# Kernel optimization log

Hardware: AMD Instinct MI355X
Metric: run time of the kernel (lower is better)

## Reference

```python
import jax, jax.numpy as jnp
import numpy as np

B, NV, NT = 256, 64, 77
UNIT_DIM, PROJ_DIM, V_HID, T_HID = 512, 512, 768, 512
TEMP_INIT = 0.07
LN_EPS = 1e-5
NORM_EPS = 1e-12


def _xavier(key, fan_in, fan_out):
    lim = np.sqrt(6.0 / (fan_in + fan_out))
    return jax.random.uniform(key, (fan_in, fan_out), jnp.float32, -lim, lim)


def _ln(x, g, b):
    mu = jnp.mean(x, axis=-1, keepdims=True)
    var = jnp.mean(jnp.square(x - mu), axis=-1, keepdims=True)
    return (x - mu) * jax.lax.rsqrt(var + LN_EPS) * g + b


def _l2norm(x):
    n = jnp.sqrt(jnp.sum(jnp.square(x), axis=-1, keepdims=True))
    return x / jnp.maximum(n, NORM_EPS)


def _unit_mlp(x, W1, b1, g, bt, W2, b2):
    # Linear -> LayerNorm -> GELU(exact) -> Linear
    h = x @ W1 + b1
    h = jax.nn.gelu(_ln(h, g, bt), approximate=False)
    return h @ W2 + b2


def setup_inputs() -> dict:
    key = jax.random.key(0)
    ks = jax.random.split(key, 12)
    inp = {
        'visual_units': jax.random.normal(ks[0], (B, NV, UNIT_DIM), jnp.float32),
        'text_units': jax.random.normal(ks[1], (B, NT, UNIT_DIM), jnp.float32),
        'visual_cls': jax.random.normal(ks[2], (B, V_HID), jnp.float32),
        'text_cls': jax.random.normal(ks[3], (B, T_HID), jnp.float32),
        # visual unit proj
        'vW1': _xavier(ks[4], UNIT_DIM, PROJ_DIM), 'vb1': jnp.zeros(PROJ_DIM),
        'vg': jnp.ones(PROJ_DIM), 'vbt': jnp.zeros(PROJ_DIM),
        'vW2': _xavier(ks[5], PROJ_DIM, PROJ_DIM), 'vb2': jnp.zeros(PROJ_DIM),
        # text unit proj
        'tW1': _xavier(ks[6], UNIT_DIM, PROJ_DIM), 'tb1': jnp.zeros(PROJ_DIM),
        'tg': jnp.ones(PROJ_DIM), 'tbt': jnp.zeros(PROJ_DIM),
        'tW2': _xavier(ks[7], PROJ_DIM, PROJ_DIM), 'tb2': jnp.zeros(PROJ_DIM),
        # global projections (Linear -> LayerNorm)
        'gvW': _xavier(ks[8], V_HID, PROJ_DIM), 'gvb': jnp.zeros(PROJ_DIM),
        'gvg': jnp.ones(PROJ_DIM), 'gvbt': jnp.zeros(PROJ_DIM),
        'gtW': _xavier(ks[9], T_HID, PROJ_DIM), 'gtb': jnp.zeros(PROJ_DIM),
        'gtg': jnp.ones(PROJ_DIM), 'gtbt': jnp.zeros(PROJ_DIM),
        'logit_scale': jnp.log(jnp.asarray(1.0 / TEMP_INIT, jnp.float32)),
    }
    return inp


def _forward(visual_units, text_units, visual_cls, text_cls,
             vW1, vb1, vg, vbt, vW2, vb2,
             tW1, tb1, tg, tbt, tW2, tb2,
             gvW, gvb, gvg, gvbt, gtW, gtb, gtg, gtbt, logit_scale):
    # unit projections, L2-normalized: [B,Nv,P], [B,Nt,P]
    v_proj = _l2norm(_unit_mlp(visual_units, vW1, vb1, vg, vbt, vW2, vb2))
    t_proj = _l2norm(_unit_mlp(text_units, tW1, tb1, tg, tbt, tW2, tb2))
    # global projections, L2-normalized: [B,P]
    v_global = _l2norm(_ln(visual_cls @ gvW + gvb, gvg, gvbt))
    t_global = _l2norm(_ln(text_cls @ gtW + gtb, gtg, gtbt))

    scale = jnp.minimum(jnp.exp(logit_scale), 100.0)

    # ---- global CLIP loss ----
    logits = scale * (v_global @ t_global.T)  # [B,B]
    diag = jnp.arange(B)
    lp_i2t = jax.nn.log_softmax(logits, axis=-1)
    lp_t2i = jax.nn.log_softmax(logits.T, axis=-1)
    loss_global = -(jnp.mean(lp_i2t[diag, diag]) + jnp.mean(lp_t2i[diag, diag])) / 2.0

    # ---- unit-level mutual-NN loss (vectorized version of the python loop) ----
    sim = jnp.einsum('bvp,btp->bvt', v_proj, t_proj) * scale  # [B,Nv,Nt]
    logp_i2t = jax.nn.log_softmax(sim, axis=-1)   # over Nt
    logp_t2i = jax.nn.log_softmax(sim, axis=-2)   # over Nv
    best_t_for_v = jnp.argmax(sim, axis=-1)       # [B,Nv]
    best_v_for_t = jnp.argmax(sim, axis=-2)       # [B,Nt]
    # mutual mask: best_v_for_t[b, best_t_for_v[b,i]] == i
    back = jnp.take_along_axis(best_v_for_t, best_t_for_v, axis=1)  # [B,Nv]
    mutual = (back == jnp.arange(NV)[None, :])                      # [B,Nv] bool
    j = best_t_for_v[..., None]                                     # [B,Nv,1]
    lp1 = jnp.take_along_axis(logp_i2t, j, axis=2)[..., 0]          # [B,Nv]
    lp2 = jnp.take_along_axis(logp_t2i, j, axis=2)[..., 0]          # [B,Nv]
    m = mutual.astype(sim.dtype)
    loss_sum = -jnp.sum(m * (lp1 + lp2))
    count = 2.0 * jnp.sum(m)  # always >= 2B: the per-sample argmax of sim is mutual
    loss_unit = loss_sum / jnp.maximum(count, 1.0)

    # ---- diversity loss ----
    def _diversity(units, n):
        u = _l2norm(units)
        s = jnp.einsum('bip,bjp->bij', u, u)
        mask = 1.0 - jnp.eye(n, dtype=s.dtype)
        return jnp.sum(jnp.abs(s) * mask) / (B * n * (n - 1))
    loss_div = (_diversity(visual_units, NV) + _diversity(text_units, NT)) / 2.0

    sim_matrix = jnp.einsum('bvp,btp->bvt', v_proj, t_proj)
    return loss_global, loss_unit, loss_div, v_proj, t_proj, v_global, t_global, sim_matrix


def reference(visual_units, text_units, visual_cls, text_cls,
              vW1, vb1, vg, vbt, vW2, vb2,
              tW1, tb1, tg, tbt, tW2, tb2,
              gvW, gvb, gvg, gvbt, gtW, gtb, gtg, gtbt, logit_scale):
    return _forward(visual_units, text_units, visual_cls, text_cls,
                    vW1, vb1, vg, vbt, vW2, vb2,
                    tW1, tb1, tg, tbt, tW2, tb2,
                    gvW, gvb, gvg, gvbt, gtW, gtb, gtg, gtbt, logit_scale)
```

## Files before the change

kernel.cpp:

```cpp
#include <hip/hip_runtime.h>
#include <math.h>

typedef __attribute__((ext_vector_type(8))) short short8;
typedef __attribute__((ext_vector_type(4))) short short4v;
typedef __attribute__((ext_vector_type(4))) float f32x4;

#define NB 256
#define NVU 64
#define NTU 77
#define PD 512

#define O_VP 3ull
#define O_TP (O_VP + (size_t)NB * NVU * PD)
#define O_VG (O_TP + (size_t)NB * NTU * PD)
#define O_TG (O_VG + (size_t)NB * PD)
#define O_SM (O_TG + (size_t)NB * PD)

#define WS_VW1T 0u
#define WS_VW2T 524288u
#define WS_TW1T 1048576u
#define WS_TW2T 1572864u
#define WS_GVWT 2097152u
#define WS_GTWT 2883584u
#define WS_LOG  3552256u
#define WS_DIAG 3814400u
#define WS_RLSE 3815424u
#define WS_CLSE 3816448u
#define WS_UP   3817472u
#define WS_UC   3818496u
#define WS_PART 3819520u
#define WS_TT   3821568u
#define WS_LOGT 4345856u

#define GL_LDS16(gp, lp) __builtin_amdgcn_global_load_lds( \
    (const __attribute__((address_space(1))) void*)(gp), \
    (__attribute__((address_space(3))) void*)(lp), 16, 0, 0)

__device__ inline short f2bf(float f) {
  union { float f; unsigned u; } v; v.f = f;
  unsigned r = v.u + 0x7FFFu + ((v.u >> 16) & 1u);
  return (short)(r >> 16);
}
__device__ inline float bf2f(short s) {
  union { unsigned u; float f; } v; v.u = ((unsigned)(unsigned short)s) << 16;
  return v.f;
}

__device__ inline float blk_sum_(float x, float* buf, int nw) {
  const int lane = threadIdx.x & 63, w = threadIdx.x >> 6;
  #pragma unroll
  for (int m = 1; m < 64; m <<= 1) x += __shfl_xor(x, m, 64);
  __syncthreads();
  if (lane == 0) buf[w] = x;
  __syncthreads();
  float s = 0.f;
  for (int i = 0; i < nw; ++i) s += buf[i];
  return s;
}
__device__ inline float blk_max_(float x, float* buf, int nw) {
  const int lane = threadIdx.x & 63, w = threadIdx.x >> 6;
  #pragma unroll
  for (int m = 1; m < 64; m <<= 1) x = fmaxf(x, __shfl_xor(x, m, 64));
  __syncthreads();
  if (lane == 0) buf[w] = x;
  __syncthreads();
  float s = buf[0];
  for (int i = 1; i < nw; ++i) s = fmaxf(s, buf[i]);
  return s;
}

__global__ __launch_bounds__(256) void k_prep(
    const float* __restrict__ s0, const float* __restrict__ s1,
    const float* __restrict__ s2, const float* __restrict__ s3,
    short* __restrict__ d0, short* __restrict__ d1,
    short* __restrict__ d2, short* __restrict__ d3,
    const float* __restrict__ gv, short* __restrict__ dv_,
    const float* __restrict__ gt, short* __restrict__ dt_) {
  __shared__ short tile[32][66];
  const int bid = blockIdx.x;
  if (bid < 512) {
    const int m = bid >> 7;
    const float* src = m == 0 ? s0 : m == 1 ? s1 : m == 2 ? s2 : s3;
    short* dst = m == 0 ? d0 : m == 1 ? d1 : m == 2 ? d2 : d3;
    const int rem = bid & 127;
    const int kc = rem >> 3, nt = rem & 7;
    const int n0 = nt * 64;
    #pragma unroll
    for (int it = 0; it < 8; ++it) {
      int idx = it * 256 + threadIdx.x;
      int r = idx >> 6, c = idx & 63;
      tile[r][c] = f2bf(src[(size_t)(kc * 32 + r) * 512 + n0 + c]);
    }
    __syncthreads();
    const int nl = threadIdx.x >> 2, s = threadIdx.x & 3;
    const int n = n0 + nl;
    short8 v;
    #pragma unroll
    for (int j = 0; j < 8; ++j) v[j] = tile[s * 8 + j][nl];
    *(short8*)&dst[(size_t)kc * 16384 + n * 32 + ((s ^ ((n >> 1) & 3)) << 3)] = v;
  } else if (bid < 2048) {
    int idx = (bid - 512) * 256 + threadIdx.x;
    int k = idx >> 9, n = idx & 511;
    dv_[(size_t)n * 768 + k] = f2bf(gv[idx]);
  } else {
    int idx = (bid - 2048) * 256 + threadIdx.x;
    int k = idx >> 9, n = idx & 511;
    dt_[(size_t)n * 512 + k] = f2bf(gt[idx]);
  }
}

__global__ __launch_bounds__(1024) void k_mega(
    const float* __restrict__ Xv, const float* __restrict__ Xt,
    const short* __restrict__ vWf1, const float* __restrict__ vb1,
    const float* __restrict__ vg, const float* __restrict__ vbt,
    const short* __restrict__ vWf2, const float* __restrict__ vb2,
    const short* __restrict__ tWf1, const float* __restrict__ tb1,
    const float* __restrict__ tg, const float* __restrict__ tbt,
    const short* __restrict__ tWf2, const float* __restrict__ tb2,
    float* __restrict__ outV, float* __restrict__ outT,
    const float* __restrict__ vsrc, const float* __restrict__ tsrc,
    const short* __restrict__ gvWT, const float* __restrict__ gvb,
    const float* __restrict__ gvg, const float* __restrict__ gvbt,
    const short* __restrict__ gtWT, const float* __restrict__ gtb,
    const float* __restrict__ gtg, const float* __restrict__ gtbt,
    float* __restrict__ outVG, float* __restrict__ outTG,
    float* __restrict__ Tt, float* __restrict__ part) {
  __shared__ __align__(16) short As[64][520];
  __shared__ __align__(16) short Bs[2][16384];
  __shared__ float redS[4][64];
  __shared__ float redQ[4][64];

  const int tid = threadIdx.x;
  const int w = tid >> 6, lane = tid & 63;
  const int hi = lane >> 4, lo = lane & 15;
  const int bid = blockIdx.x;

  if (bid < 564) {
    const int rg = w >> 2, cg = w & 3;
    const int xcd = bid & 7, ii = bid >> 3;
    const int orig = (xcd < 4 ? xcd * 71 : 284 + (xcd - 4) * 70) + ii;
    const bool isv = orig < 256;
    const int rb = isv ? orig : orig - 256;
    const float* __restrict__ X   = isv ? Xv : Xt;
    const short* __restrict__ Wf1 = isv ? vWf1 : tWf1;
    const float* __restrict__ b1  = isv ? vb1  : tb1;
    const float* __restrict__ gg  = isv ? vg   : tg;
    const float* __restrict__ bt  = isv ? vbt  : tbt;
    const short* __restrict__ Wf2 = isv ? vWf2 : tWf2;
    const float* __restrict__ b2  = isv ? vb2  : tb2;
    float* __restrict__ outF      = isv ? outV : outT;
    const size_t row0 = (size_t)rb * 64;

    const int arow = rg * 16 + lo;
    const int bswz = (cg * 128 + lo) * 32 + ((hi ^ ((lo >> 1) & 3)) * 8);

    GL_LDS16(Wf1 + tid * 8, &Bs[0][tid * 8]);
    GL_LDS16(Wf1 + 8192 + tid * 8, &Bs[0][8192 + tid * 8]);

    const f32x4* Xp = (const f32x4*)(X + row0 * 512);
    #pragma unroll
    for (int i = 0; i < 8; ++i) {
      int idx = i * 1024 + tid;
      f32x4 f = __builtin_nontemporal_load(Xp + idx);
      short4v s4 = {f2bf(f[0]), f2bf(f[1]), f2bf(f[2]), f2bf(f[3])};
      *(short4v*)&As[idx >> 7][(idx & 127) * 4] = s4;
    }
    __syncthreads();

    f32x4 acc[8];
    #pragma unroll
    for (int ct = 0; ct < 8; ++ct) acc[ct] = (f32x4){0.f, 0.f, 0.f, 0.f};

    GL_LDS16(Wf1 + 16384 + tid * 8, &Bs[1][tid * 8]);
    GL_LDS16(Wf1 + 16384 + 8192 + tid * 8, &Bs[1][8192 + tid * 8]);

    for (int kc = 0; kc < 16; ++kc) {
      const int cur = kc & 1;
      short8 a = *(const short8*)&As[arow][kc * 32 + hi * 8];
      #pragma unroll
      for (int ct = 0; ct < 8; ++ct) {
        short8 bb = *(const short8*)&Bs[cur][bswz + ct * 512];
        acc[ct] = __builtin_amdgcn_mfma_f32_16x16x32_bf16(a, bb, acc[ct], 0, 0, 0);
      }
      __builtin_amdgcn_s_barrier();
      const int nc = kc + 2;
      const short* nxt = (nc < 16) ? (Wf1 + (size_t)nc * 16384)
                                   : (Wf2 + (size_t)(nc - 16) * 16384);
      GL_LDS16(nxt + tid * 8, &Bs[cur][tid * 8]);
      GL_LDS16(nxt + 8192 + tid * 8, &Bs[cur][8192 + tid * 8]);
      asm volatile("s_waitcnt vmcnt(2)" ::: "memory");
    }

    {
      float ps[4] = {0.f, 0.f, 0.f, 0.f}, pq[4] = {0.f, 0.f, 0.f, 0.f};
      #pragma unroll
      for (int ct = 0; ct < 8; ++ct) {
        float bia = b1[cg * 128 + ct * 16 + lo];
        #pragma unroll
        for (int r = 0; r < 4; ++r) {
          float v = acc[ct][r] + bia;
          acc[ct][r] = v;
          ps[r] += v; pq[r] += v * v;
        }
      }
      #pragma unroll
      for (int m = 1; m < 16; m <<= 1)
        #pragma unroll
        for (int r = 0; r < 4; ++r) {
          ps[r] += __shfl_xor(ps[r], m, 64);
          pq[r] += __shfl_xor(pq[r], m, 64);
        }
      if (lo == 0) {
        #pragma unroll
        for (int r = 0; r < 4; ++r) {
          int rr = rg * 16 + hi * 4 + r;
          redS[cg][rr] = ps[r]; redQ[cg][rr] = pq[r];
        }
      }
    }
    __syncthreads();

    {
      float mu[4], rs[4];
      #pragma unroll
      for (int r = 0; r < 4; ++r) {
        int rr = rg * 16 + hi * 4 + r;
        float s = redS[0][rr] + redS[1][rr] + redS[2][rr] + redS[3][rr];
        float q = redQ[0][rr] + redQ[1][rr] + redQ[2][rr] + redQ[3][rr];
        float m_ = s * (1.f / 512.f);
        mu[r] = m_;
        rs[r] = rsqrtf(q * (1.f / 512.f) - m_ * m_ + 1e-5f);
      }
      #pragma unroll
      for (int ct = 0; ct < 8; ++ct) {
        int col = cg * 128 + ct * 16 + lo;
        float ga = gg[col], be = bt[col];
        #pragma unroll
        for (int r = 0; r < 4; ++r) {
          float xn = (acc[ct][r] - mu[r]) * rs[r] * ga + be;
          float ge = 0.5f * xn * (1.f + erff(xn * 0.70710678118654752f));
          As[rg * 16 + hi * 4 + r][col] = f2bf(ge);
        }
      }
    }
    __syncthreads();

    #pragma unroll
    for (int ct = 0; ct < 8; ++ct) acc[ct] = (f32x4){0.f, 0.f, 0.f, 0.f};
    for (int kc = 0; kc < 16; ++kc) {
      const int cur = kc & 1;
      short8 a = *(const short8*)&As[arow][kc * 32 + hi * 8];
      #pragma unroll
      for (int ct = 0; ct < 8; ++ct) {
        short8 bb = *(const short8*)&Bs[cur][bswz + ct * 512];
        acc[ct] = __builtin_amdgcn_mfma_f32_16x16x32_bf16(a, bb, acc[ct], 0, 0, 0);
      }
      __builtin_amdgcn_s_barrier();
      if (kc < 14) {
        const short* nxt = Wf2 + (size_t)(kc + 2) * 16384;
        GL_LDS16(nxt + tid * 8, &Bs[cur][tid * 8]);
        GL_LDS16(nxt + 8192 + tid * 8, &Bs[cur][8192 + tid * 8]);
        asm volatile("s_waitcnt vmcnt(2)" ::: "memory");
      } else if (kc == 14) {
        asm volatile("s_waitcnt vmcnt(0)" ::: "memory");
      }
    }

    {
      float pq[4] = {0.f, 0.f, 0.f, 0.f};
      #pragma unroll
      for (int ct = 0; ct < 8; ++ct) {
        float bia = b2[cg * 128 + ct * 16 + lo];
        #pragma unroll
        for (int r = 0; r < 4; ++r) {
          float v = acc[ct][r] + bia;
          acc[ct][r] = v;
          pq[r] += v * v;
        }
      }
      #pragma unroll
      for (int m = 1; m < 16; m <<= 1)
        #pragma unroll
        for (int r = 0; r < 4; ++r) pq[r] += __shfl_xor(pq[r], m, 64);
      if (lo == 0) {
        #pragma unroll
        for (int r = 0; r < 4; ++r) redQ[cg][rg * 16 + hi * 4 + r] = pq[r];
      }
    }
    __syncthreads();
    {
      float invn[4];
      #pragma unroll
      for (int r = 0; r < 4; ++r) {
        int rr = rg * 16 + hi * 4 + r;
        float q = redQ[0][rr] + redQ[1][rr] + redQ[2][rr] + redQ[3][rr];
        invn[r] = 1.f / fmaxf(sqrtf(q), 1e-12f);
      }
      #pragma unroll
      for (int ct = 0; ct < 8; ++ct) {
        int col = cg * 128 + ct * 16 + lo;
        #pragma unroll
        for (int r = 0; r < 4; ++r)
          outF[(row0 + rg * 16 + hi * 4 + r) * 512 + col] = acc[ct][r] * invn[r];
      }
    }
  } else if (bid < 1076) {
    float* srow = (float*)&As[0][0];
    float* rb = &redS[0][0];
    const int row = bid - 564;
    const bool isv = row < 256;
    const int r2 = row & 255;
    const int K = isv ? 768 : 512;
    const float* src = isv ? vsrc : tsrc;
    const short* WT = isv ? gvWT : gtWT;
    const float* bias = isv ? gvb : gtb;
    const float* gg = isv ? gvg : gtg;
    const float* bt = isv ? gvbt : gtbt;
    float* outp = isv ? outVG : outTG;
    const bool act = tid < 256;

    for (int k = tid; k < K; k += 1024) srow[k] = src[(size_t)r2 * K + k];
    __syncthreads();
    float v0 = 0.f, v1 = 0.f;
    if (act) {
      const short* wp0 = WT + (size_t)tid * K;
      const short* wp1 = WT + (size_t)(tid + 256) * K;
      for (int k = 0; k < K; k += 8) {
        short8 wa = *(const short8*)(wp0 + k);
        short8 wb = *(const short8*)(wp1 + k);
        #pragma unroll
        for (int j = 0; j < 8; ++j) {
          float sv = srow[k + j];
          v0 += sv * bf2f(wa[j]);
          v1 += sv * bf2f(wb[j]);
        }
      }
      v0 += bias[tid]; v1 += bias[tid + 256];
    }
    float s = act ? (v0 + v1) : 0.f;
    float q = act ? (v0 * v0 + v1 * v1) : 0.f;
    #pragma unroll
    for (int m = 1; m < 64; m <<= 1) {
      s += __shfl_xor(s, m, 64);
      q += __shfl_xor(q, m, 64);
    }
    if (lane == 0 && w < 4) { rb[w] = s; rb[4 + w] = q; }
    __syncthreads();
    s = rb[0] + rb[1] + rb[2] + rb[3];
    q = rb[4] + rb[5] + rb[6] + rb[7];
    __syncthreads();
    float mu = s * (1.f / 512.f);
    float var = q * (1.f / 512.f) - mu * mu;
    float rs = rsqrtf(var + 1e-5f);
    float y0 = 0.f, y1 = 0.f;
    if (act) {
      y0 = (v0 - mu) * rs * gg[tid] + bt[tid];
      y1 = (v1 - mu) * rs * gg[tid + 256] + bt[tid + 256];
    }
    float ss = act ? (y0 * y0 + y1 * y1) : 0.f;
    #pragma unroll
    for (int m = 1; m < 64; m <<= 1) ss += __shfl_xor(ss, m, 64);
    if (lane == 0 && w < 4) rb[w] = ss;
    __syncthreads();
    ss = rb[0] + rb[1] + rb[2] + rb[3];
    float invn = 1.f / fmaxf(sqrtf(ss), 1e-12f);
    if (act) {
      float o0 = y0 * invn, o1 = y1 * invn;
      outp[(size_t)r2 * 512 + tid] = o0;
      outp[(size_t)r2 * 512 + tid + 256] = o1;
      if (!isv) {
        Tt[(size_t)tid * 256 + r2] = o0;
        Tt[(size_t)(tid + 256) * 256 + r2] = o1;
      }
    }
  } else {
    short (*Bsd)[136] = (short(*)[136])&As[0][0];
    float* invs = &redQ[0][0];
    float* rbuf5 = &redS[0][0];
    const int sub = bid - 1076;
    const bool isv = sub < 256;
    const int b = sub & 255;
    const int N = isv ? 64 : 77;
    const float* X = (isv ? Xv : Xt) + (size_t)b * N * 512;
    const int ri = w * 16 + lo;

    f32x4 acc[5];
    #pragma unroll
    for (int ct = 0; ct < 5; ++ct) acc[ct] = (f32x4){0.f, 0.f, 0.f, 0.f};

    for (int c = 0; c < 4; ++c) {
      for (int s5 = tid; s5 < 80 * 32; s5 += 1024) {
        int r = s5 >> 5, cgp = s5 & 31;
        short4v s4 = {0, 0, 0, 0};
        if (r < N) {
          float4 f = *(const float4*)(X + (size_t)r * 512 + c * 128 + cgp * 4);
          s4 = (short4v){f2bf(f.x), f2bf(f.y), f2bf(f.z), f2bf(f.w)};
        }
        *(short4v*)&Bsd[r][cgp * 4] = s4;
      }
      __syncthreads();
      if (tid < 320) {
        #pragma unroll
        for (int kc = 0; kc < 4; ++kc) {
          short8 a = *(const short8*)&Bsd[ri][kc * 32 + hi * 8];
          #pragma unroll
          for (int ct = 0; ct < 5; ++ct) {
            short8 bb = *(const short8*)&Bsd[ct * 16 + lo][kc * 32 + hi * 8];
            acc[ct] = __builtin_amdgcn_mfma_f32_16x16x32_bf16(a, bb, acc[ct], 0, 0, 0);
          }
        }
      }
      __syncthreads();
    }

    if (tid < 320) {
      #pragma unroll
      for (int ct = 0; ct < 5; ++ct)
        #pragma unroll
        for (int r = 0; r < 4; ++r) {
          int i = w * 16 + hi * 4 + r, j = ct * 16 + lo;
          if (i == j && i < N) invs[i] = 1.f / fmaxf(sqrtf(fmaxf(acc[ct][r], 0.f)), 1e-12f);
        }
    }
    __syncthreads();

    float cs = 0.f;
    if (tid < 320) {
      #pragma unroll
      for (int ct = 0; ct < 5; ++ct)
        #pragma unroll
        for (int r = 0; r < 4; ++r) {
          int i = w * 16 + hi * 4 + r, j = ct * 16 + lo;
          if (i < N && j < N && i != j)
            cs += fabsf(acc[ct][r]) * invs[i] * invs[j];
        }
    }
    #pragma unroll
    for (int m = 1; m < 64; m <<= 1) cs += __shfl_xor(cs, m, 64);
    if (lane == 0 && w < 5) rbuf5[w] = cs;
    __syncthreads();
    if (tid == 0) {
      float s = 0.f;
      for (int i = 0; i < 5; ++i) s += rbuf5[i];
      part[sub] = s;
    }
  }
}

__global__ __launch_bounds__(256) void k_logits_row(
    const float* __restrict__ vgp, const float* __restrict__ Tt,
    const float* __restrict__ lsc, float* __restrict__ logits,
    float* __restrict__ logitsT,
    float* __restrict__ diag, float* __restrict__ rlse) {
  __shared__ __align__(16) float vrow[512];
  __shared__ float rbuf[4];
  const int i = blockIdx.x, tid = threadIdx.x;
  const float scale = fminf(expf(lsc[0]), 100.f);
  vrow[tid] = vgp[(size_t)i * 512 + tid];
  vrow[tid + 256] = vgp[(size_t)i * 512 + 256 + tid];
  __syncthreads();
  float s = 0.f;
  #pragma unroll 8
  for (int k = 0; k < 512; ++k)
    s += vrow[k] * Tt[(size_t)k * 256 + tid];
  float lg = scale * s;
  logits[(size_t)i * 256 + tid] = lg;
  logitsT[(size_t)tid * 256 + i] = lg;
  if (tid == i) diag[i] = lg;
  float mx = blk_max_(lg, rbuf, 4);
  float se = blk_sum_(expf(lg - mx), rbuf, 4);
  if (tid == 0) rlse[i] = mx + logf(se);
}

__global__ __launch_bounds__(256) void k_logits_col(
    const float* __restrict__ logitsT, float* __restrict__ clse) {
  __shared__ float rbuf[4];
  const int j = blockIdx.x, tid = threadIdx.x;
  float lg = logitsT[(size_t)j * 256 + tid];
  float mx = blk_max_(lg, rbuf, 4);
  float se = blk_sum_(expf(lg - mx), rbuf, 4);
  if (tid == 0) clse[j] = mx + logf(se);
}

__global__ __launch_bounds__(512) void k_unit_sim(
    const float* __restrict__ vpp, const float* __restrict__ tpp,
    const float* __restrict__ lsc, float* __restrict__ simout,
    float* __restrict__ up, float* __restrict__ uc) {
  __shared__ float Sp[2][64][81];
  __shared__ float lse_r[64];
  __shared__ int bestt[64];
  __shared__ float lse_c[80];
  __shared__ int bestv[80];
  __shared__ float rbuf[8];
  const int b = blockIdx.x;
  const int tid = threadIdx.x;
  const int w = tid >> 6, lane = tid & 63;
  const int wq = w >> 1, kg = w & 1;
  const int hi = lane >> 4, lo = lane & 15;
  const float scale = fminf(expf(lsc[0]), 100.f);

  f32x4 acc[5];
  #pragma unroll
  for (int ct = 0; ct < 5; ++ct) acc[ct] = (f32x4){0.f, 0.f, 0.f, 0.f};

  const float* va = vpp + ((size_t)b * 64 + wq * 16 + lo) * 512 + kg * 256;
  const float* tbase = tpp + (size_t)b * 77 * 512 + kg * 256;
  for (int k0 = 0; k0 < 256; k0 += 32) {
    float4 f0 = *(const float4*)(va + k0 + hi * 8);
    float4 f1 = *(const float4*)(va + k0 + hi * 8 + 4);
    short8 a = {f2bf(f0.x), f2bf(f0.y), f2bf(f0.z), f2bf(f0.w),
                f2bf(f1.x), f2bf(f1.y), f2bf(f1.z), f2bf(f1.w)};
    #pragma unroll
    for (int ct = 0; ct < 5; ++ct) {
      int rj = ct * 16 + lo;
      short8 bb = {0, 0, 0, 0, 0, 0, 0, 0};
      if (rj < 77) {
        const float* tb = tbase + (size_t)rj * 512 + k0 + hi * 8;
        float4 g0 = *(const float4*)tb;
        float4 g1 = *(const float4*)(tb + 4);
        bb = (short8){f2bf(g0.x), f2bf(g0.y), f2bf(g0.z), f2bf(g0.w),
                      f2bf(g1.x), f2bf(g1.y), f2bf(g1.z), f2bf(g1.w)};
      }
      acc[ct] = __builtin_amdgcn_mfma_f32_16x16x32_bf16(a, bb, acc[ct], 0, 0, 0);
    }
  }
  #pragma unroll
  for (int ct = 0; ct < 5; ++ct)
    #pragma unroll
    for (int r = 0; r < 4; ++r) {
      int i = wq * 16 + hi * 4 + r, j = ct * 16 + lo;
      if (j < 77) Sp[kg][i][j] = acc[ct][r];
    }
  __syncthreads();
  for (int idx = tid; idx < 64 * 77; idx += 512) {
    int i = idx / 77, j = idx - i * 77;
    float s = Sp[0][i][j] + Sp[1][i][j];
    simout[((size_t)b * 64 + i) * 77 + j] = s;
    Sp[0][i][j] = s * scale;
  }
  __syncthreads();
  if (tid < 64) {
    float mx = -1e30f; int am = 0;
    for (int t = 0; t < 77; ++t) { float x = Sp[0][tid][t]; if (x > mx) { mx = x; am = t; } }
    float se = 0.f;
    for (int t = 0; t < 77; ++t) se += expf(Sp[0][tid][t] - mx);
    lse_r[tid] = mx + logf(se); bestt[tid] = am;
  } else if (tid < 64 + 77) {
    int t = tid - 64;
    float mx = -1e30f; int am = 0;
    for (int v = 0; v < 64; ++v) { float x = Sp[0][v][t]; if (x > mx) { mx = x; am = v; } }
    float se = 0.f;
    for (int v = 0; v < 64; ++v) se += expf(Sp[0][v][t] - mx);
    lse_c[t] = mx + logf(se); bestv[t] = am;
  }
  __syncthreads();
  float c = 0.f, cnt = 0.f;
  if (tid < 64) {
    int j = bestt[tid];
    if (bestv[j] == tid) {
      float sv = Sp[0][tid][j];
      c = -((sv - lse_r[tid]) + (sv - lse_c[j]));
      cnt = 2.f;
    }
  }
  c = blk_sum_(c, rbuf, 8);
  cnt = blk_sum_(cnt, rbuf, 8);
  if (tid == 0) { up[b] = c; uc[b] = cnt; }
}

__global__ __launch_bounds__(256) void k_final(
    const float* __restrict__ diag, const float* __restrict__ rlse,
    const float* __restrict__ clse, const float* __restrict__ up,
    const float* __restrict__ uc, const float* __restrict__ part,
    float* __restrict__ out) {
  __shared__ float rbuf[4];
  const int tid = threadIdx.x;
  float d = diag[tid];
  float s1 = blk_sum_(d - rlse[tid], rbuf, 4);
  float s2 = blk_sum_(d - clse[tid], rbuf, 4);
  float su = blk_sum_(up[tid], rbuf, 4);
  float sc = blk_sum_(uc[tid], rbuf, 4);
  float sv = blk_sum_(part[tid], rbuf, 4);
  float st = blk_sum_(part[tid + 256], rbuf, 4);
  if (tid == 0) {
    out[0] = -(s1 * (1.f / 256.f) + s2 * (1.f / 256.f)) * 0.5f;
    out[1] = su / fmaxf(sc, 1.f);
    out[2] = (sv / (256.f * 64.f * 63.f) + st / (256.f * 77.f * 76.f)) * 0.5f;
  }
}

extern "C" void kernel_launch(void* const* d_in, const int* in_sizes, int n_in,
                              void* d_out, int out_size, void* d_ws, size_t ws_size,
                              hipStream_t stream) {
  const float* vis_units = (const float*)d_in[0];
  const float* txt_units = (const float*)d_in[1];
  const float* vis_cls = (const float*)d_in[2];
  const float* txt_cls = (const float*)d_in[3];
  const float* vW1 = (const float*)d_in[4];
  const float* vb1 = (const float*)d_in[5];
  const float* vg  = (const float*)d_in[6];
  const float* vbt = (const float*)d_in[7];
  const float* vW2 = (const float*)d_in[8];
  const float* vb2 = (const float*)d_in[9];
  const float* tW1 = (const float*)d_in[10];
  const float* tb1 = (const float*)d_in[11];
  const float* tg  = (const float*)d_in[12];
  const float* tbt = (const float*)d_in[13];
  const float* tW2 = (const float*)d_in[14];
  const float* tb2 = (const float*)d_in[15];
  const float* gvW = (const float*)d_in[16];
  const float* gvb = (const float*)d_in[17];
  const float* gvg = (const float*)d_in[18];
  const float* gvbt = (const float*)d_in[19];
  const float* gtW = (const float*)d_in[20];
  const float* gtb = (const float*)d_in[21];
  const float* gtg = (const float*)d_in[22];
  const float* gtbt = (const float*)d_in[23];
  const float* lsc = (const float*)d_in[24];

  float* out = (float*)d_out;
  char* ws = (char*)d_ws;
  short* vW1T = (short*)(ws + WS_VW1T);
  short* vW2T = (short*)(ws + WS_VW2T);
  short* tW1T = (short*)(ws + WS_TW1T);
  short* tW2T = (short*)(ws + WS_TW2T);
  short* gvWT = (short*)(ws + WS_GVWT);
  short* gtWT = (short*)(ws + WS_GTWT);
  float* logits = (float*)(ws + WS_LOG);
  float* diag = (float*)(ws + WS_DIAG);
  float* rlse = (float*)(ws + WS_RLSE);
  float* clse = (float*)(ws + WS_CLSE);
  float* up = (float*)(ws + WS_UP);
  float* uc = (float*)(ws + WS_UC);
  float* part = (float*)(ws + WS_PART);
  float* Tt = (float*)(ws + WS_TT);
  float* logitsT = (float*)(ws + WS_LOGT);

  k_prep<<<3072, 256, 0, stream>>>(vW1, vW2, tW1, tW2, vW1T, vW2T, tW1T, tW2T,
                                   gvW, gvWT, gtW, gtWT);

  k_mega<<<1588, 1024, 0, stream>>>(
      vis_units, txt_units,
      vW1T, vb1, vg, vbt, vW2T, vb2,
      tW1T, tb1, tg, tbt, tW2T, tb2,
      out + O_VP, out + O_TP,
      vis_cls, txt_cls,
      gvWT, gvb, gvg, gvbt, gtWT, gtb, gtg, gtbt,
      out + O_VG, out + O_TG, Tt, part);

  k_logits_row<<<256, 256, 0, stream>>>(out + O_VG, Tt, lsc, logits, logitsT, diag, rlse);
  k_logits_col<<<256, 256, 0, stream>>>(logitsT, clse);

  k_unit_sim<<<256, 512, 0, stream>>>(out + O_VP, out + O_TP, lsc, out + O_SM, up, uc);

  k_final<<<1, 256, 0, stream>>>(diag, rlse, clse, up, uc, part, out);

  (void)in_sizes; (void)n_in; (void)out_size; (void)ws_size;
}
```

Baseline: 230.2 us.

## Fuse visual diversity Gram into unit-MLP blocks; pair text diversity per block

The visual-unit MLP blocks already hold a 64-row bf16 tile of the visual units in LDS, so the visual diversity Gram matrix is now computed there with 16 waves, each taking one 16x16 tile. This removes the separate visual diversity blocks and their reload and conversion of the inputs from global memory. Text diversity blocks now each process two batches in sequence, which cuts the grid from 1588 to 1204 blocks. The cost is extra work and two barriers on the critical path of the visual MLP blocks, and text diversity blocks that run about twice as long.

```diff
diff --git a/kernel.cpp b/kernel.cpp
--- a/kernel.cpp
+++ b/kernel.cpp
@@ -167,12 +167,42 @@
     }
     __syncthreads();
 
-    f32x4 acc[8];
-    #pragma unroll
-    for (int ct = 0; ct < 8; ++ct) acc[ct] = (f32x4){0.f, 0.f, 0.f, 0.f};
-
     GL_LDS16(Wf1 + 16384 + tid * 8, &Bs[1][tid * 8]);
     GL_LDS16(Wf1 + 16384 + 8192 + tid * 8, &Bs[1][8192 + tid * 8]);
+
+    if (isv) {
+      const int ti = rg, tj = cg;
+      f32x4 g = (f32x4){0.f, 0.f, 0.f, 0.f};
+      for (int kc = 0; kc < 16; ++kc) {
+        short8 ga = *(const short8*)&As[ti * 16 + lo][kc * 32 + hi * 8];
+        short8 gb = *(const short8*)&As[tj * 16 + lo][kc * 32 + hi * 8];
+        g = __builtin_amdgcn_mfma_f32_16x16x32_bf16(ga, gb, g, 0, 0, 0);
+      }
+      float* invs = &redQ[0][0];
+      if (ti == tj && (lo >> 2) == hi)
+        invs[ti * 16 + lo] = 1.f / fmaxf(sqrtf(fmaxf(g[lo & 3], 0.f)), 1e-12f);
+      __syncthreads();
+      float cs = 0.f;
+      #pragma unroll
+      for (int r = 0; r < 4; ++r) {
+        int i = ti * 16 + hi * 4 + r, j = tj * 16 + lo;
+        if (i != j) cs += fabsf(g[r]) * invs[i] * invs[j];
+      }
+      #pragma unroll
+      for (int m = 1; m < 64; m <<= 1) cs += __shfl_xor(cs, m, 64);
+      if (lane == 0) redS[0][w] = cs;
+      __syncthreads();
+      if (tid == 0) {
+        float s = 0.f;
+        #pragma unroll
+        for (int i = 0; i < 16; ++i) s += redS[0][i];
+        part[rb] = s;
+      }
+    }
+
+    f32x4 acc[8];
+    #pragma unroll
+    for (int ct = 0; ct < 8; ++ct) acc[ct] = (f32x4){0.f, 0.f, 0.f, 0.f};
 
     for (int kc = 0; kc < 16; ++kc) {
       const int cur = kc & 1;
@@ -304,10 +334,80 @@
           outF[(row0 + rg * 16 + hi * 4 + r) * 512 + col] = acc[ct][r] * invn[r];
       }
     }
-  } else if (bid < 1076) {
+  } else if (bid < 692) {
+    short (*Bsd)[136] = (short(*)[136])&As[0][0];
+    float* invs = &redQ[0][0];
+    float* rbuf5 = &redS[0][0];
+    const int ri = w * 16 + lo;
+    for (int half = 0; half < 2; ++half) {
+      const int b = (bid - 564) * 2 + half;
+      const float* X = Xt + (size_t)b * NTU * 512;
+      f32x4 acc[5];
+      #pragma unroll
+      for (int ct = 0; ct < 5; ++ct) acc[ct] = (f32x4){0.f, 0.f, 0.f, 0.f};
+
+      for (int c = 0; c < 4; ++c) {
+        for (int s5 = tid; s5 < 80 * 32; s5 += 1024) {
+          int r = s5 >> 5, cgp = s5 & 31;
+          short4v s4 = {0, 0, 0, 0};
+          if (r < NTU) {
+            float4 f = *(const float4*)(X + (size_t)r * 512 + c * 128 + cgp * 4);
+            s4 = (short4v){f2bf(f.x), f2bf(f.y), f2bf(f.z), f2bf(f.w)};
+          }
+          *(short4v*)&Bsd[r][cgp * 4] = s4;
+        }
+        __syncthreads();
+        if (tid < 320) {
+          #pragma unroll
+          for (int kc = 0; kc < 4; ++kc) {
+            short8 a = *(const short8*)&Bsd[ri][kc * 32 + hi * 8];
+            #pragma unroll
+            for (int ct = 0; ct < 5; ++ct) {
+              short8 bb = *(const short8*)&Bsd[ct * 16 + lo][kc * 32 + hi * 8];
+              acc[ct] = __builtin_amdgcn_mfma_f32_16x16x32_bf16(a, bb, acc[ct], 0, 0, 0);
+            }
+          }
+        }
+        __syncthreads();
+      }
+
+      if (tid < 320) {
+        #pragma unroll
+        for (int ct = 0; ct < 5; ++ct)
+          #pragma unroll
+          for (int r = 0; r < 4; ++r) {
+            int i = w * 16 + hi * 4 + r, j = ct * 16 + lo;
+            if (i == j && i < NTU) invs[i] = 1.f / fmaxf(sqrtf(fmaxf(acc[ct][r], 0.f)), 1e-12f);
+          }
+      }
+      __syncthreads();
+
+      float cs = 0.f;
+      if (tid < 320) {
+        #pragma unroll
+        for (int ct = 0; ct < 5; ++ct)
+          #pragma unroll
+          for (int r = 0; r < 4; ++r) {
+            int i = w * 16 + hi * 4 + r, j = ct * 16 + lo;
+            if (i < NTU && j < NTU && i != j)
+              cs += fabsf(acc[ct][r]) * invs[i] * invs[j];
+          }
+      }
+      #pragma unroll
+      for (int m = 1; m < 64; m <<= 1) cs += __shfl_xor(cs, m, 64);
+      if (lane == 0 && w < 5) rbuf5[w] = cs;
+      __syncthreads();
+      if (tid == 0) {
+        float s = 0.f;
+        for (int i = 0; i < 5; ++i) s += rbuf5[i];
+        part[256 + b] = s;
+      }
+      __syncthreads();
+    }
+  } else {
     float* srow = (float*)&As[0][0];
     float* rb = &redS[0][0];
-    const int row = bid - 564;
+    const int row = bid - 692;
     const bool isv = row < 256;
     const int r2 = row & 255;
     const int K = isv ? 768 : 512;
@@ -372,77 +472,6 @@
         Tt[(size_t)tid * 256 + r2] = o0;
         Tt[(size_t)(tid + 256) * 256 + r2] = o1;
       }
-    }
-  } else {
-    short (*Bsd)[136] = (short(*)[136])&As[0][0];
-    float* invs = &redQ[0][0];
-    float* rbuf5 = &redS[0][0];
-    const int sub = bid - 1076;
-    const bool isv = sub < 256;
-    const int b = sub & 255;
-    const int N = isv ? 64 : 77;
-    const float* X = (isv ? Xv : Xt) + (size_t)b * N * 512;
-    const int ri = w * 16 + lo;
-
-    f32x4 acc[5];
-    #pragma unroll
-    for (int ct = 0; ct < 5; ++ct) acc[ct] = (f32x4){0.f, 0.f, 0.f, 0.f};
-
-    for (int c = 0; c < 4; ++c) {
-      for (int s5 = tid; s5 < 80 * 32; s5 += 1024) {
-        int r = s5 >> 5, cgp = s5 & 31;
-        short4v s4 = {0, 0, 0, 0};
-        if (r < N) {
-          float4 f = *(const float4*)(X + (size_t)r * 512 + c * 128 + cgp * 4);
-          s4 = (short4v){f2bf(f.x), f2bf(f.y), f2bf(f.z), f2bf(f.w)};
-        }
-        *(short4v*)&Bsd[r][cgp * 4] = s4;
-      }
-      __syncthreads();
-      if (tid < 320) {
-        #pragma unroll
-        for (int kc = 0; kc < 4; ++kc) {
-          short8 a = *(const short8*)&Bsd[ri][kc * 32 + hi * 8];
-          #pragma unroll
-          for (int ct = 0; ct < 5; ++ct) {
-            short8 bb = *(const short8*)&Bsd[ct * 16 + lo][kc * 32 + hi * 8];
-            acc[ct] = __builtin_amdgcn_mfma_f32_16x16x32_bf16(a, bb, acc[ct], 0, 0, 0);
-          }
-        }
-      }
-      __syncthreads();
-    }
-
-    if (tid < 320) {
-      #pragma unroll
-      for (int ct = 0; ct < 5; ++ct)
-        #pragma unroll
-        for (int r = 0; r < 4; ++r) {
-          int i = w * 16 + hi * 4 + r, j = ct * 16 + lo;
-          if (i == j && i < N) invs[i] = 1.f / fmaxf(sqrtf(fmaxf(acc[ct][r], 0.f)), 1e-12f);
-        }
-    }
-    __syncthreads();
-
-    float cs = 0.f;
-    if (tid < 320) {
-      #pragma unroll
-      for (int ct = 0; ct < 5; ++ct)
-        #pragma unroll
-        for (int r = 0; r < 4; ++r) {
-          int i = w * 16 + hi * 4 + r, j = ct * 16 + lo;
-          if (i < N && j < N && i != j)
-            cs += fabsf(acc[ct][r]) * invs[i] * invs[j];
-        }
-    }
-    #pragma unroll
-    for (int m = 1; m < 64; m <<= 1) cs += __shfl_xor(cs, m, 64);
-    if (lane == 0 && w < 5) rbuf5[w] = cs;
-    __syncthreads();
-    if (tid == 0) {
-      float s = 0.f;
-      for (int i = 0; i < 5; ++i) s += rbuf5[i];
-      part[sub] = s;
     }
   }
 }
@@ -639,7 +668,7 @@
   k_prep<<<3072, 256, 0, stream>>>(vW1, vW2, tW1, tW2, vW1T, vW2T, tW1T, tW2T,
                                    gvW, gvWT, gtW, gtWT);
 
-  k_mega<<<1588, 1024, 0, stream>>>(
+  k_mega<<<1204, 1024, 0, stream>>>(
       vis_units, txt_units,
       vW1T, vb1, vg, vbt, vW2T, vb2,
       tW1T, tb1, tg, tbt, tW2T, tb2,
```

Result: no change. 230.2 us, median of 2 (+0.0%).
